# Performance work log

Measured on AMD Instinct MI355X. Metric: run time of the kernel, lower is better.

The kernel has to match this reference:

```python
import jax, jax.numpy as jnp
import numpy as np

B, C, H, W = 2, 192, 128, 128
DG, K = 4, 9  # deformable groups, kernel taps (3x3)


def conv3x3(x, w, b):
    y = jax.lax.conv_general_dilated(x, w, (1, 1), ((1, 1), (1, 1)),
                                     dimension_numbers=('NCHW', 'OIHW', 'NCHW'))
    return y + b[None, :, None, None]


def deform_sample(x, dy, dx, mask):
    # x: [B,C,H,W]; dy,dx,mask: [B,DG,K,H,W]. Returns [B,C,K,H,W] masked bilinear samples.
    b, c, h, w = x.shape
    cg = c // DG
    kk = jnp.arange(K)
    ky = (kk // 3 - 1).astype(x.dtype)  # kernel row offsets {-1,0,1}, pad=1, stride=1
    kx = (kk % 3 - 1).astype(x.dtype)
    ii = jnp.arange(h, dtype=x.dtype)
    jj = jnp.arange(w, dtype=x.dtype)
    py = ii[None, None, None, :, None] + ky[None, None, :, None, None] + dy  # [B,DG,K,H,W]
    px = jj[None, None, None, None, :] + kx[None, None, :, None, None] + dx
    y0 = jnp.floor(py)
    x0 = jnp.floor(px)
    ly = py - y0
    lx = px - x0
    xf = x.reshape(b, DG, cg, h * w)
    out = jnp.zeros((b, DG, cg, K, h, w), dtype=x.dtype)
    corners = [(y0, x0, (1 - ly) * (1 - lx)), (y0, x0 + 1, (1 - ly) * lx),
               (y0 + 1, x0, ly * (1 - lx)), (y0 + 1, x0 + 1, ly * lx)]
    for yc, xc, wt in corners:
        valid = (yc >= 0) & (yc < h) & (xc >= 0) & (xc < w)  # zero padding outside
        wv = wt * valid.astype(x.dtype)
        idx = (jnp.clip(yc, 0, h - 1) * w + jnp.clip(xc, 0, w - 1)).astype(jnp.int32)
        idxb = jnp.broadcast_to(idx.reshape(b, DG, 1, K * h * w), (b, DG, cg, K * h * w))
        g = jnp.take_along_axis(xf, idxb, axis=3).reshape(b, DG, cg, K, h, w)
        out = out + wv[:, :, None] * g
    out = out * mask[:, :, None]
    return out.reshape(b, c, K, h, w)


def setup_inputs() -> dict:
    key = jax.random.key(0)
    ks = jax.random.split(key, 8)
    f32 = jnp.float32
    x_vq = jax.random.normal(ks[0], (B, C, H, W), f32)
    x_residual = jax.random.normal(ks[1], (B, C, H, W), f32)
    w_off = jax.random.normal(ks[2], (C, 2 * C, 3, 3), f32) * (1.0 / np.sqrt(2 * C * 9))
    b_off = jnp.zeros((C,), f32)
    # conv_offset of DCNv2Pack: C -> 3*DG*K channels; small init keeps offsets moderate
    w_co = jax.random.normal(ks[3], (3 * DG * K, C, 3, 3), f32) * 0.02
    b_co = jnp.zeros((3 * DG * K,), f32)
    w_dcn = jax.random.normal(ks[4], (C, C, 3, 3), f32) * (1.0 / np.sqrt(C * 9))
    b_dcn = jnp.zeros((C,), f32)
    return {"x_vq": x_vq, "x_residual": x_residual, "w_off": w_off, "b_off": b_off,
            "w_co": w_co, "b_co": b_co, "w_dcn": w_dcn, "b_dcn": b_dcn}


def reference(x_vq, x_residual, w_off, b_off, w_co, b_co, w_dcn, b_dcn):
    feat = conv3x3(jnp.concatenate([x_vq, x_residual], axis=1), w_off, b_off)  # [B,C,H,W]
    off_out = conv3x3(feat, w_co, b_co)  # [B,3*DG*K,H,W]
    gk = DG * K
    o1 = off_out[:, :gk]
    o2 = off_out[:, gk:2 * gk]
    mask = jax.nn.sigmoid(off_out[:, 2 * gk:])
    dy = o1.reshape(B, DG, K, H, W)
    dx = o2.reshape(B, DG, K, H, W)
    m = mask.reshape(B, DG, K, H, W)
    sampled = deform_sample(x_vq, dy, dx, m)  # [B,C,K,H,W]
    y = jnp.einsum('ock,bckhw->bohw', w_dcn.reshape(C, C, K), sampled)
    return y + b_dcn[None, :, None, None]
```

## Files before the change

kernel.cpp:

```cpp
#include <hip/hip_runtime.h>
#include <hip/hip_bf16.h>
#include <math.h>

#define HH 128
#define WW 128
#define HW 16384
#define BB 2
#define CC 192

typedef __attribute__((ext_vector_type(8)))  short short8;
typedef __attribute__((ext_vector_type(4)))  float f32x4;
typedef __attribute__((ext_vector_type(16))) float f32x16;
typedef __attribute__((ext_vector_type(2)))  float f32x2;
typedef __attribute__((ext_vector_type(4)))  unsigned u32x4;

static __device__ __forceinline__ short f2bf(float f) {
    unsigned u = __float_as_uint(f);
    unsigned r = (u + 0x7FFFu + ((u >> 16) & 1u)) >> 16;
    return (short)r;
}
static __device__ __forceinline__ f32x2 unpk(unsigned u) {
    f32x2 r;
    r[0] = __uint_as_float(u << 16);
    r[1] = __uint_as_float(u & 0xFFFF0000u);
    return r;
}

static __device__ __forceinline__ void gl_lds16(const short* gsrc, short* ldst) {
    __builtin_amdgcn_global_load_lds(
        (const __attribute__((address_space(1))) unsigned*)gsrc,
        (__attribute__((address_space(3))) unsigned*)ldst, 16, 0, 0);
}

__global__ __launch_bounds__(256) void to_grp_k(
    const float* __restrict__ xv, const float* __restrict__ xr,
    unsigned short* __restrict__ xg)
{
    const int idx = blockIdx.x * 256 + threadIdx.x;
    const int pos = idx & (HW - 1);
    const int cgb = idx >> 14;
    const int cg  = cgb % 48;
    const int b   = cgb / 48;
    short8 v;
#pragma unroll
    for (int r = 0; r < 8; r++) {
        const int c = cg * 8 + r;
        const float f = (c < 192)
            ? xv[((size_t)(b * 192 + c) << 14) + pos]
            : xr[((size_t)(b * 192 + (c - 192)) << 14) + pos];
        v[r] = f2bf(f);
    }
    *reinterpret_cast<short8*>(xg + (size_t)idx * 8) = v;
}

__global__ void pack_w_k(const float* __restrict__ w, short* __restrict__ wp,
                         int Co, int so, int d1, int s1, int d2, int s2, int s3,
                         int total)
{
    const int idx = blockIdx.x * blockDim.x + threadIdx.x;
    if (idx >= total) return;
    const int lane  = idx & 63;
    const int slot  = (idx >> 6) & 7;
    const int chunk = idx >> 9;
    const int o     = slot * 32 + (lane & 31);
    const int k0    = chunk * 16 + ((lane >> 5) << 3);
    short8 v;
#pragma unroll
    for (int r = 0; r < 8; r++) {
        const int k = k0 + r;
        float f = 0.f;
        if (o < Co) {
            const int rem = k % d1;
            f = w[(size_t)o * so + (k / d1) * s1 + (rem / d2) * s2 + (rem % d2) * s3];
        }
        v[r] = f2bf(f);
    }
    *reinterpret_cast<short8*>(wp + (size_t)idx * 8) = v;
}

template<int MTW, int NC16, bool OUT_GRP>
__global__ __launch_bounds__(256, 2) void conv_g_k(
    const unsigned short* __restrict__ xg,
    const short* __restrict__ wA, const float* __restrict__ bias,
    void* __restrict__ outp, int Cout)
{
    __shared__ __align__(16) short Pbuf[3][2][4096];

    const int t    = threadIdx.x;
    const int lane = t & 63;
    const int wid  = t >> 6;
    const int mg   = wid >> 1;
    const int nt   = wid & 1;
    const int lin  = (blockIdx.z * HH + blockIdx.y) * 2 + blockIdx.x;
    const int og_  = (lin & 7) * 64 + (lin >> 3);
    const int j0   = (og_ & 1) * 64;
    const int i    = (og_ >> 1) & (HH - 1);
    const int b    = og_ >> 8;
    const int px   = j0 + (nt << 5) + (lane & 31);
    const int hi   = lane >> 5;
    constexpr int NQ = NC16 * 9;
    constexpr int NP = NQ / 2;

    const unsigned short* __restrict__ xgb = xg + (size_t)b * (NC16 * 2) * HW * 8;

    f32x16 acc[MTW];
#pragma unroll
    for (int m = 0; m < MTW; m++)
#pragma unroll
        for (int r = 0; r < 16; r++) acc[m][r] = 0.f;

    auto loadB = [&](int qq, short8& dst, bool& vm) {
        const int c16 = qq / 9;
        const int tap = qq - c16 * 9;
        const int iy  = i + tap / 3 - 1;
        const int jx  = px + tap % 3 - 1;
        vm = ((unsigned)iy < HH) && ((unsigned)jx < WW);
        const int iyc = min(max(iy, 0), HH - 1);
        const int jxc = min(max(jx, 0), WW - 1);
        dst = *reinterpret_cast<const short8*>(
            xgb + ((size_t)(c16 * 2 + hi) * HW + (iyc << 7) + jxc) * 8);
    };
    auto stage2 = [&](int chunk, int pb, int sl) {
        gl_lds16(wA + (size_t)chunk * 4096 + t * 8,         &Pbuf[pb][sl][wid * 512]);
        gl_lds16(wA + (size_t)chunk * 4096 + (t + 256) * 8, &Pbuf[pb][sl][2048 + wid * 512]);
    };

    short8 B0, B1, B2, B3, B4, B5;
    bool M0, M1, M2, M3, M4, M5;

    stage2(0, 0, 0); stage2(1, 0, 1);
    loadB(0, B0, M0); loadB(1, B1, M1);
    stage2(2, 1, 0); stage2(3, 1, 1);
    loadB(2, B2, M2); loadB(3, B3, M3);

#define CCHUNK(IBUF, SL, BC, MC)                                              \
    {                                                                         \
        short8 bF = BC;                                                       \
        if (!MC) {                                                            \
            _Pragma("unroll")                                                 \
            for (int r = 0; r < 8; r++) bF[r] = 0;                            \
        }                                                                     \
        const short* ab_ = &Pbuf[IBUF][SL][(mg * MTW) * 512 + lane * 8];      \
        short8 aF[MTW];                                                       \
        _Pragma("unroll")                                                     \
        for (int m = 0; m < MTW; m++)                                         \
            aF[m] = *reinterpret_cast<const short8*>(ab_ + m * 512);          \
        __builtin_amdgcn_s_setprio(1);                                        \
        _Pragma("unroll")                                                     \
        for (int m = 0; m < MTW; m++)                                         \
            acc[m] = __builtin_amdgcn_mfma_f32_32x32x16_bf16(aF[m], bF, acc[m], 0, 0, 0); \
        __builtin_amdgcn_s_setprio(0);                                        \
    }

#define PSTEP(P, IBUF, SBUF, Bc0, Mc0, Bc1, Mc1, Bn0, Mn0, Bn1, Mn1)          \
    {                                                                         \
        loadB(min(2 * ((P) + 2),     NQ - 1), Bn0, Mn0);                      \
        loadB(min(2 * ((P) + 2) + 1, NQ - 1), Bn1, Mn1);                      \
        asm volatile("s_waitcnt vmcnt(8)" ::: "memory");                      \
        __builtin_amdgcn_s_barrier();                                         \
        __builtin_amdgcn_sched_barrier(0);                                    \
        const int sc0_ = min(2 * ((P) + 2),     NQ - 1);                      \
        const int sc1_ = min(2 * ((P) + 2) + 1, NQ - 1);                      \
        stage2(sc0_, SBUF, 0); stage2(sc1_, SBUF, 1);                         \
        CCHUNK(IBUF, 0, Bc0, Mc0);                                            \
        CCHUNK(IBUF, 1, Bc1, Mc1);                                            \
    }

    for (int pp = 0; pp < NP; pp += 3) {
        PSTEP(pp + 0, 0, 2, B0, M0, B1, M1, B4, M4, B5, M5);
        PSTEP(pp + 1, 1, 0, B2, M2, B3, M3, B0, M0, B1, M1);
        PSTEP(pp + 2, 2, 1, B4, M4, B5, M5, B2, M2, B3, M3);
    }
#undef PSTEP
#undef CCHUNK

    const int pos_o = (i << 7) + px;
    if constexpr (OUT_GRP) {
        unsigned short* fg = (unsigned short*)outp;
#pragma unroll
        for (int m = 0; m < MTW; m++) {
            const int mt32 = mg * MTW + m;
#pragma unroll
            for (int g = 0; g < 4; g++) {
                const int ob = mt32 * 32 + 8 * g + 4 * hi;
                const unsigned s0 = (unsigned short)f2bf(acc[m][4 * g + 0] + bias[ob + 0]);
                const unsigned s1 = (unsigned short)f2bf(acc[m][4 * g + 1] + bias[ob + 1]);
                const unsigned s2 = (unsigned short)f2bf(acc[m][4 * g + 2] + bias[ob + 2]);
                const unsigned s3 = (unsigned short)f2bf(acc[m][4 * g + 3] + bias[ob + 3]);
                const int cg = mt32 * 4 + g;
                *reinterpret_cast<uint2*>(
                    fg + ((size_t)(b * (Cout >> 3) + cg) * HW + pos_o) * 8 + 4 * hi) =
                    make_uint2(s0 | (s1 << 16), s2 | (s3 << 16));
            }
        }
    } else {
        float* of = (float*)outp;
#pragma unroll
        for (int m = 0; m < MTW; m++) {
            const int mt32 = mg * MTW + m;
#pragma unroll
            for (int reg = 0; reg < 16; reg++) {
                const int o = mt32 * 32 + (reg & 3) + ((reg >> 2) << 3) + (hi << 2);
                if (o < Cout)
                    of[((size_t)(b * Cout + o) << 14) + pos_o] = acc[m][reg] + bias[o];
            }
        }
    }
}

__global__ __launch_bounds__(128, 2) void dcn_g_k(
    const unsigned short* __restrict__ xg, const float* __restrict__ off,
    const short* __restrict__ wA, const float* __restrict__ bias,
    float* __restrict__ out)
{
    __shared__ __align__(16) f32x4 eW[1152];
    __shared__ __align__(8)  uint2 eO[1152];
    __shared__ __align__(16) short bfS[2][2][512];

    const int t    = threadIdx.x;
    const int lane = t & 63;
    const int w    = t >> 6;
    const int lin  = (blockIdx.z * HH + blockIdx.y) * 4 + blockIdx.x;
    const int og_  = (lin & 7) * 128 + (lin >> 3);
    const int jt   = og_ & 3;
    const int i    = (og_ >> 2) & (HH - 1);
    const int b    = og_ >> 9;
    const int j0   = jt * 32;

    for (int e = t; e < 1152; e += 128) {
        const int p  = e & 31;
        const int gk = e >> 5;
        const int kt = gk % 9;
        const int j  = j0 + p;
        const size_t sp = (size_t)b * 108 * HW + (size_t)gk * HW + (i << 7) + j;
        const float dy = off[sp];
        const float dx = off[sp + (size_t)36 * HW];
        const float mv = off[sp + (size_t)72 * HW];
        const float m  = 1.f / (1.f + expf(-mv));
        const float py = (float)(i + kt / 3 - 1) + dy;
        const float px = (float)(j + kt % 3 - 1) + dx;
        const float y0f = floorf(py), x0f = floorf(px);
        const float ly = py - y0f, lx = px - x0f;
        const int y0 = (int)y0f, x0 = (int)x0f;
        const float vy0 = (y0 >= 0 && y0 < HH) ? 1.f : 0.f;
        const float vy1 = (y0 + 1 >= 0 && y0 + 1 < HH) ? 1.f : 0.f;
        const float vx0 = (x0 >= 0 && x0 < WW) ? 1.f : 0.f;
        const float vx1 = (x0 + 1 >= 0 && x0 + 1 < WW) ? 1.f : 0.f;
        f32x4 w4;
        w4[0] = (1.f - ly) * (1.f - lx) * m * vy0 * vx0;
        w4[1] = (1.f - ly) * lx         * m * vy0 * vx1;
        w4[2] = ly         * (1.f - lx) * m * vy1 * vx0;
        w4[3] = ly         * lx         * m * vy1 * vx1;
        const int yc0 = min(max(y0, 0), HH - 1);
        const int yc1 = min(max(y0 + 1, 0), HH - 1);
        const int xc0 = min(max(x0, 0), WW - 1);
        const int xc1 = min(max(x0 + 1, 0), WW - 1);
        eW[e] = w4;
        eO[e] = make_uint2((unsigned)((yc0 << 7) + xc0) | ((unsigned)((yc0 << 7) + xc1) << 16),
                           (unsigned)((yc1 << 7) + xc0) | ((unsigned)((yc1 << 7) + xc1) << 16));
    }
    __syncthreads();

    const int px_l = lane & 31;
    const int hi   = lane >> 5;
    const unsigned short* __restrict__ xgb = xg + (size_t)b * 48 * HW * 8;

    f32x16 acc[3];
#pragma unroll
    for (int m = 0; m < 3; m++)
#pragma unroll
        for (int r = 0; r < 16; r++) acc[m][r] = 0.f;

#define GISSUE(QQ, N0, N1, N2, N3, WN)                                        \
    {                                                                         \
        const int qn_   = min((QQ), 107);                                     \
        const int c16n_ = qn_ / 9;                                            \
        const int ktn_  = qn_ - 9 * c16n_;                                    \
        const int e_    = ((c16n_ / 3) * 9 + ktn_) * 32 + px_l;               \
        const uint2 o_  = eO[e_];                                             \
        WN = eW[e_];                                                          \
        const unsigned short* base_ = xgb + (size_t)(c16n_ * 2 + hi) * (HW * 8); \
        N0 = *reinterpret_cast<const u32x4*>(base_ + (size_t)(o_.x & 0xFFFFu) * 8); \
        N1 = *reinterpret_cast<const u32x4*>(base_ + (size_t)(o_.x >> 16) * 8);     \
        N2 = *reinterpret_cast<const u32x4*>(base_ + (size_t)(o_.y & 0xFFFFu) * 8); \
        N3 = *reinterpret_cast<const u32x4*>(base_ + (size_t)(o_.y >> 16) * 8);     \
    }

#define AISSUE(PP, DST)                                                       \
    {                                                                         \
        const short* a0_ = wA + (size_t)min(2 * (PP),     107) * 4096 + (w * 3) * 512 + lane * 8; \
        const short* a1_ = wA + (size_t)min(2 * (PP) + 1, 107) * 4096 + (w * 3) * 512 + lane * 8; \
        DST[0] = *reinterpret_cast<const short8*>(a0_);                       \
        DST[1] = *reinterpret_cast<const short8*>(a0_ + 512);                 \
        DST[2] = *reinterpret_cast<const short8*>(a0_ + 1024);                \
        DST[3] = *reinterpret_cast<const short8*>(a1_);                       \
        DST[4] = *reinterpret_cast<const short8*>(a1_ + 512);                 \
        DST[5] = *reinterpret_cast<const short8*>(a1_ + 1024);                \
    }

#define PAIRSTEP(P, Ac, C0, C1, C2, C3, WC, An, N0, N1, N2, N3, WN)           \
    {                                                                         \
        GISSUE(2 * ((P) + 1) + w, N0, N1, N2, N3, WN);                        \
        AISSUE((P) + 1, An);                                                  \
        asm volatile("s_waitcnt vmcnt(10)" ::: "memory");                     \
        u32x4 rv_;                                                            \
        _Pragma("unroll")                                                     \
        for (int jj = 0; jj < 4; jj++) {                                      \
            f32x2 v_ = WC[0] * unpk(C0[jj]) + WC[1] * unpk(C1[jj])            \
                     + WC[2] * unpk(C2[jj]) + WC[3] * unpk(C3[jj]);           \
            __hip_bfloat162 h2_ = __float22bfloat162_rn(make_float2(v_[0], v_[1])); \
            unsigned hu_; __builtin_memcpy(&hu_, &h2_, 4);                    \
            rv_[jj] = hu_;                                                    \
        }                                                                     \
        *reinterpret_cast<u32x4*>(&bfS[(P) & 1][w][lane * 8]) = rv_;          \
        asm volatile("s_waitcnt lgkmcnt(0)" ::: "memory");                    \
        __builtin_amdgcn_s_barrier();                                         \
        __builtin_amdgcn_sched_barrier(0);                                    \
        const short8 bf0_ = *reinterpret_cast<const short8*>(&bfS[(P) & 1][0][lane * 8]); \
        const short8 bf1_ = *reinterpret_cast<const short8*>(&bfS[(P) & 1][1][lane * 8]); \
        __builtin_amdgcn_s_setprio(1);                                        \
        acc[0] = __builtin_amdgcn_mfma_f32_32x32x16_bf16(Ac[0], bf0_, acc[0], 0, 0, 0); \
        acc[1] = __builtin_amdgcn_mfma_f32_32x32x16_bf16(Ac[1], bf0_, acc[1], 0, 0, 0); \
        acc[2] = __builtin_amdgcn_mfma_f32_32x32x16_bf16(Ac[2], bf0_, acc[2], 0, 0, 0); \
        acc[0] = __builtin_amdgcn_mfma_f32_32x32x16_bf16(Ac[3], bf1_, acc[0], 0, 0, 0); \
        acc[1] = __builtin_amdgcn_mfma_f32_32x32x16_bf16(Ac[4], bf1_, acc[1], 0, 0, 0); \
        acc[2] = __builtin_amdgcn_mfma_f32_32x32x16_bf16(Ac[5], bf1_, acc[2], 0, 0, 0); \
        __builtin_amdgcn_s_setprio(0);                                        \
    }

    short8 Aa[6], Ab[6];
    u32x4 Gx0, Gx1, Gx2, Gx3, Gy0, Gy1, Gy2, Gy3;
    f32x4 wGx, wGy;

    GISSUE(0 + w, Gx0, Gx1, Gx2, Gx3, wGx);
    AISSUE(0, Aa);

    for (int pr = 0; pr < 54; pr += 2) {
        PAIRSTEP(pr,     Aa, Gx0, Gx1, Gx2, Gx3, wGx, Ab, Gy0, Gy1, Gy2, Gy3, wGy);
        PAIRSTEP(pr + 1, Ab, Gy0, Gy1, Gy2, Gy3, wGy, Aa, Gx0, Gx1, Gx2, Gx3, wGx);
    }
#undef PAIRSTEP
#undef AISSUE
#undef GISSUE

    const int pos_o = (i << 7) + j0 + px_l;
#pragma unroll
    for (int m = 0; m < 3; m++) {
        const int mt32 = w * 3 + m;
#pragma unroll
        for (int reg = 0; reg < 16; reg++) {
            const int o = mt32 * 32 + (reg & 3) + ((reg >> 2) << 3) + (hi << 2);
            out[((size_t)(b * CC + o) << 14) + pos_o] = acc[m][reg] + bias[o];
        }
    }
}

extern "C" void kernel_launch(void* const* d_in, const int* in_sizes, int n_in,
                              void* d_out, int out_size, void* d_ws, size_t ws_size,
                              hipStream_t stream)
{
    const float* x_vq  = (const float*)d_in[0];
    const float* x_res = (const float*)d_in[1];
    const float* w_off = (const float*)d_in[2];
    const float* b_off = (const float*)d_in[3];
    const float* w_co  = (const float*)d_in[4];
    const float* b_co  = (const float*)d_in[5];
    const float* w_dcn = (const float*)d_in[6];
    const float* b_dcn = (const float*)d_in[7];
    float* out = (float*)d_out;

    char* ws = (char*)d_ws;
    unsigned short* xg = (unsigned short*)ws;
    const size_t xg_sz = (size_t)BB * 48 * HW * 8 * 2;
    unsigned short* fg = (unsigned short*)(ws + xg_sz);
    const size_t fg_sz = (size_t)BB * 24 * HW * 8 * 2;
    float* offb = (float*)(ws + xg_sz + fg_sz);
    const size_t offb_sz = (size_t)BB * 108 * HW * 4;
    short* wA1 = (short*)(ws + xg_sz + fg_sz + offb_sz);
    short* wA2 = wA1 + (size_t)216 * 4096;
    short* wA3 = wA2 + (size_t)108 * 4096;

    to_grp_k<<<dim3(BB * 48 * HW / 256), 256, 0, stream>>>(x_vq, x_res, xg);

    pack_w_k<<<(216 * 512 + 255) / 256, 256, 0, stream>>>(
        w_off, wA1, 192, 3456, 144, 144, 16, 1, 9, 216 * 512);
    pack_w_k<<<(108 * 512 + 255) / 256, 256, 0, stream>>>(
        w_co, wA2, 108, 1728, 144, 144, 16, 1, 9, 108 * 512);
    pack_w_k<<<(108 * 512 + 255) / 256, 256, 0, stream>>>(
        w_dcn, wA3, 192, 1728, 144, 144, 16, 1, 9, 108 * 512);

    conv_g_k<3, 24, true><<<dim3(2, HH, BB), 256, 0, stream>>>(xg, wA1, b_off, fg, 192);
    conv_g_k<2, 12, false><<<dim3(2, HH, BB), 256, 0, stream>>>(fg, wA2, b_co, offb, 108);
    dcn_g_k<<<dim3(4, HH, BB), 128, 0, stream>>>(xg, offb, wA3, b_dcn, out);
}
```

Measured before the change: 174.2 us.

## Stage conv input halo tile in LDS instead of per-tap global loads

```diff
diff --git a/kernel.cpp b/kernel.cpp
--- a/kernel.cpp
+++ b/kernel.cpp
@@ -26,7 +26,7 @@
     return r;
 }
 
-static __device__ __forceinline__ void gl_lds16(const short* gsrc, short* ldst) {
+static __device__ __forceinline__ void gl_lds16(const void* gsrc, void* ldst) {
     __builtin_amdgcn_global_load_lds(
         (const __attribute__((address_space(1))) unsigned*)gsrc,
         (__attribute__((address_space(3))) unsigned*)ldst, 16, 0, 0);
@@ -85,6 +85,7 @@
     void* __restrict__ outp, int Cout)
 {
     __shared__ __align__(16) short Pbuf[3][2][4096];
+    __shared__ __align__(16) short Btile[2][4096];
 
     const int t    = threadIdx.x;
     const int lane = t & 63;
@@ -96,12 +97,13 @@
     const int j0   = (og_ & 1) * 64;
     const int i    = (og_ >> 1) & (HH - 1);
     const int b    = og_ >> 8;
-    const int px   = j0 + (nt << 5) + (lane & 31);
+    const int pxw  = (nt << 5) + (lane & 31);
     const int hi   = lane >> 5;
     constexpr int NQ = NC16 * 9;
     constexpr int NP = NQ / 2;
 
     const unsigned short* __restrict__ xgb = xg + (size_t)b * (NC16 * 2) * HW * 8;
+    const char* __restrict__ xgc = (const char*)xgb;
 
     f32x16 acc[MTW];
 #pragma unroll
@@ -109,34 +111,45 @@
 #pragma unroll
         for (int r = 0; r < 16; r++) acc[m][r] = 0.f;
 
-    auto loadB = [&](int qq, short8& dst, bool& vm) {
-        const int c16 = qq / 9;
-        const int tap = qq - c16 * 9;
-        const int iy  = i + tap / 3 - 1;
-        const int jx  = px + tap % 3 - 1;
-        vm = ((unsigned)iy < HH) && ((unsigned)jx < WW);
-        const int iyc = min(max(iy, 0), HH - 1);
-        const int jxc = min(max(jx, 0), WW - 1);
-        dst = *reinterpret_cast<const short8*>(
-            xgb + ((size_t)(c16 * 2 + hi) * HW + (iyc << 7) + jxc) * 8);
+    int spat[2], hib[2];
+#pragma unroll
+    for (int p = 0; p < 2; p++) {
+        const int off = p * 4096 + t * 16;
+        int rn = off / 1056; rn = rn > 5 ? 5 : rn;
+        const int wi  = off - rn * 1056;
+        const int h_  = rn >= 3 ? 1 : 0;
+        const int row = rn - 3 * h_;
+        const int gy  = min(max(i - 1 + row, 0), HH - 1);
+        spat[p] = ((gy << 7) + j0 - 1) * 16 + wi;
+        hib[p]  = h_;
+    }
+    auto stageB = [&](int nb) {
+        char* dstb = (char*)&Btile[nb & 1][0];
+#pragma unroll
+        for (int p = 0; p < 2; p++) {
+            const char* src = xgc + (size_t)(nb * 2 + hib[p]) * (HW * 16) + spat[p];
+            gl_lds16(src, dstb + p * 4096 + wid * 1024);
+        }
     };
     auto stage2 = [&](int chunk, int pb, int sl) {
         gl_lds16(wA + (size_t)chunk * 4096 + t * 8,         &Pbuf[pb][sl][wid * 512]);
         gl_lds16(wA + (size_t)chunk * 4096 + (t + 256) * 8, &Pbuf[pb][sl][2048 + wid * 512]);
     };
 
-    short8 B0, B1, B2, B3, B4, B5;
-    bool M0, M1, M2, M3, M4, M5;
-
     stage2(0, 0, 0); stage2(1, 0, 1);
-    loadB(0, B0, M0); loadB(1, B1, M1);
+    stageB(0);
     stage2(2, 1, 0); stage2(3, 1, 1);
-    loadB(2, B2, M2); loadB(3, B3, M3);
-
-#define CCHUNK(IBUF, SL, BC, MC)                                              \
+
+#define CCHUNK(IBUF, SL, Q)                                                   \
     {                                                                         \
-        short8 bF = BC;                                                       \
-        if (!MC) {                                                            \
+        const int cc16_ = (Q) / 9;                                            \
+        const int tap_  = (Q) - 9 * cc16_;                                    \
+        const int dy_ = tap_ / 3, dx_ = tap_ % 3;                             \
+        const int iy_ = i + dy_ - 1;                                          \
+        const int jx_ = j0 + pxw + dx_ - 1;                                   \
+        short8 bF = *reinterpret_cast<const short8*>(                         \
+            &Btile[cc16_ & 1][(hi * 3 + dy_) * 528 + (pxw + dx_) * 8]);       \
+        if (!(((unsigned)iy_ < HH) && ((unsigned)jx_ < WW))) {                \
             _Pragma("unroll")                                                 \
             for (int r = 0; r < 8; r++) bF[r] = 0;                            \
         }                                                                     \
@@ -152,29 +165,30 @@
         __builtin_amdgcn_s_setprio(0);                                        \
     }
 
-#define PSTEP(P, IBUF, SBUF, Bc0, Mc0, Bc1, Mc1, Bn0, Mn0, Bn1, Mn1)          \
+#define PSTEP(P, IBUF, SBUF)                                                  \
     {                                                                         \
-        loadB(min(2 * ((P) + 2),     NQ - 1), Bn0, Mn0);                      \
-        loadB(min(2 * ((P) + 2) + 1, NQ - 1), Bn1, Mn1);                      \
-        asm volatile("s_waitcnt vmcnt(8)" ::: "memory");                      \
+        asm volatile("s_waitcnt vmcnt(4)" ::: "memory");                      \
         __builtin_amdgcn_s_barrier();                                         \
         __builtin_amdgcn_sched_barrier(0);                                    \
-        const int sc0_ = min(2 * ((P) + 2),     NQ - 1);                      \
-        const int sc1_ = min(2 * ((P) + 2) + 1, NQ - 1);                      \
-        stage2(sc0_, SBUF, 0); stage2(sc1_, SBUF, 1);                         \
-        CCHUNK(IBUF, 0, Bc0, Mc0);                                            \
-        CCHUNK(IBUF, 1, Bc1, Mc1);                                            \
+        const int q0_  = 2 * (P);                                             \
+        const int c16_ = q0_ / 9;                                             \
+        const int t0_  = q0_ - 9 * c16_;                                      \
+        if (t0_ == 1 || t0_ == 2) stageB(min(c16_ + 1, NC16 - 1));            \
+        stage2(min(2 * ((P) + 2),     NQ - 1), SBUF, 0);                      \
+        stage2(min(2 * ((P) + 2) + 1, NQ - 1), SBUF, 1);                      \
+        CCHUNK(IBUF, 0, q0_);                                                 \
+        CCHUNK(IBUF, 1, q0_ + 1);                                             \
     }
 
     for (int pp = 0; pp < NP; pp += 3) {
-        PSTEP(pp + 0, 0, 2, B0, M0, B1, M1, B4, M4, B5, M5);
-        PSTEP(pp + 1, 1, 0, B2, M2, B3, M3, B0, M0, B1, M1);
-        PSTEP(pp + 2, 2, 1, B4, M4, B5, M5, B2, M2, B3, M3);
+        PSTEP(pp + 0, 0, 2);
+        PSTEP(pp + 1, 1, 0);
+        PSTEP(pp + 2, 2, 1);
     }
 #undef PSTEP
 #undef CCHUNK
 
-    const int pos_o = (i << 7) + px;
+    const int pos_o = (i << 7) + j0 + pxw;
     if constexpr (OUT_GRP) {
         unsigned short* fg = (unsigned short*)outp;
 #pragma unroll
@@ -370,13 +384,13 @@
     float* out = (float*)d_out;
 
     char* ws = (char*)d_ws;
-    unsigned short* xg = (unsigned short*)ws;
+    unsigned short* xg = (unsigned short*)(ws + 256);
     const size_t xg_sz = (size_t)BB * 48 * HW * 8 * 2;
-    unsigned short* fg = (unsigned short*)(ws + xg_sz);
+    unsigned short* fg = (unsigned short*)(ws + 256 + xg_sz);
     const size_t fg_sz = (size_t)BB * 24 * HW * 8 * 2;
-    float* offb = (float*)(ws + xg_sz + fg_sz);
+    float* offb = (float*)(ws + 256 + xg_sz + fg_sz);
     const size_t offb_sz = (size_t)BB * 108 * HW * 4;
-    short* wA1 = (short*)(ws + xg_sz + fg_sz + offb_sz);
+    short* wA1 = (short*)(ws + 256 + xg_sz + fg_sz + offb_sz);
     short* wA2 = wA1 + (size_t)216 * 4096;
     short* wA3 = wA2 + (size_t)108 * 4096;
 
```

Result: slower. 205.4 us (+17.9%).

## Split conv blocks by output-channel half and shrink to 128 threads

Applied to the files above, without the earlier changes.

```diff
diff --git a/kernel.cpp b/kernel.cpp
--- a/kernel.cpp
+++ b/kernel.cpp
@@ -26,7 +26,7 @@
     return r;
 }
 
-static __device__ __forceinline__ void gl_lds16(const short* gsrc, short* ldst) {
+static __device__ __forceinline__ void gl_lds16(const void* gsrc, void* ldst) {
     __builtin_amdgcn_global_load_lds(
         (const __attribute__((address_space(1))) unsigned*)gsrc,
         (__attribute__((address_space(3))) unsigned*)ldst, 16, 0, 0);
@@ -55,13 +55,13 @@
 
 __global__ void pack_w_k(const float* __restrict__ w, short* __restrict__ wp,
                          int Co, int so, int d1, int s1, int d2, int s2, int s3,
-                         int total)
+                         int SLOTS, int total)
 {
     const int idx = blockIdx.x * blockDim.x + threadIdx.x;
     if (idx >= total) return;
     const int lane  = idx & 63;
-    const int slot  = (idx >> 6) & 7;
-    const int chunk = idx >> 9;
+    const int slot  = (idx >> 6) % SLOTS;
+    const int chunk = (idx >> 6) / SLOTS;
     const int o     = slot * 32 + (lane & 31);
     const int k0    = chunk * 16 + ((lane >> 5) << 3);
     short8 v;
@@ -79,25 +79,26 @@
 }
 
 template<int MTW, int NC16, bool OUT_GRP>
-__global__ __launch_bounds__(256, 2) void conv_g_k(
+__global__ __launch_bounds__(128, 2) void conv_g_k(
     const unsigned short* __restrict__ xg,
     const short* __restrict__ wA, const float* __restrict__ bias,
     void* __restrict__ outp, int Cout)
 {
-    __shared__ __align__(16) short Pbuf[3][2][4096];
+    constexpr int NPASS   = (MTW >= 3) ? 2 : 1;
+    constexpr int SLOT_SH = NPASS * 1024;
+    __shared__ __align__(16) short Pbuf[3][2][SLOT_SH];
 
     const int t    = threadIdx.x;
     const int lane = t & 63;
     const int wid  = t >> 6;
-    const int mg   = wid >> 1;
-    const int nt   = wid & 1;
-    const int lin  = (blockIdx.z * HH + blockIdx.y) * 2 + blockIdx.x;
-    const int og_  = (lin & 7) * 64 + (lin >> 3);
-    const int j0   = (og_ & 1) * 64;
-    const int i    = (og_ >> 1) & (HH - 1);
-    const int b    = og_ >> 8;
-    const int px   = j0 + (nt << 5) + (lane & 31);
-    const int hi   = lane >> 5;
+    const int lin   = (blockIdx.z * HH + blockIdx.y) * 4 + blockIdx.x;
+    const int og_   = (lin & 7) * 128 + (lin >> 3);
+    const int chalf = og_ & 1;
+    const int pxh   = (og_ >> 1) & 1;
+    const int i     = (og_ >> 2) & (HH - 1);
+    const int b     = og_ >> 9;
+    const int px    = pxh * 64 + (wid << 5) + (lane & 31);
+    const int hi    = lane >> 5;
     constexpr int NQ = NC16 * 9;
     constexpr int NP = NQ / 2;
 
@@ -120,17 +121,19 @@
         dst = *reinterpret_cast<const short8*>(
             xgb + ((size_t)(c16 * 2 + hi) * HW + (iyc << 7) + jxc) * 8);
     };
-    auto stage2 = [&](int chunk, int pb, int sl) {
-        gl_lds16(wA + (size_t)chunk * 4096 + t * 8,         &Pbuf[pb][sl][wid * 512]);
-        gl_lds16(wA + (size_t)chunk * 4096 + (t + 256) * 8, &Pbuf[pb][sl][2048 + wid * 512]);
+    auto stageA = [&](int chunk, int pb, int sl) {
+        const short* src = wA + (size_t)chunk * (2 * MTW * 512) + chalf * (MTW * 512);
+#pragma unroll
+        for (int p = 0; p < NPASS; p++)
+            gl_lds16(src + p * 1024 + t * 8, &Pbuf[pb][sl][p * 1024 + wid * 512]);
     };
 
     short8 B0, B1, B2, B3, B4, B5;
     bool M0, M1, M2, M3, M4, M5;
 
-    stage2(0, 0, 0); stage2(1, 0, 1);
+    stageA(0, 0, 0); stageA(1, 0, 1);
     loadB(0, B0, M0); loadB(1, B1, M1);
-    stage2(2, 1, 0); stage2(3, 1, 1);
+    stageA(2, 1, 0); stageA(3, 1, 1);
     loadB(2, B2, M2); loadB(3, B3, M3);
 
 #define CCHUNK(IBUF, SL, BC, MC)                                              \
@@ -140,7 +143,7 @@
             _Pragma("unroll")                                                 \
             for (int r = 0; r < 8; r++) bF[r] = 0;                            \
         }                                                                     \
-        const short* ab_ = &Pbuf[IBUF][SL][(mg * MTW) * 512 + lane * 8];      \
+        const short* ab_ = &Pbuf[IBUF][SL][lane * 8];                         \
         short8 aF[MTW];                                                       \
         _Pragma("unroll")                                                     \
         for (int m = 0; m < MTW; m++)                                         \
@@ -156,12 +159,15 @@
     {                                                                         \
         loadB(min(2 * ((P) + 2),     NQ - 1), Bn0, Mn0);                      \
         loadB(min(2 * ((P) + 2) + 1, NQ - 1), Bn1, Mn1);                      \
-        asm volatile("s_waitcnt vmcnt(8)" ::: "memory");                      \
+        if constexpr (NPASS == 2) {                                           \
+            asm volatile("s_waitcnt vmcnt(8)" ::: "memory");                  \
+        } else {                                                              \
+            asm volatile("s_waitcnt vmcnt(6)" ::: "memory");                  \
+        }                                                                     \
         __builtin_amdgcn_s_barrier();                                         \
         __builtin_amdgcn_sched_barrier(0);                                    \
-        const int sc0_ = min(2 * ((P) + 2),     NQ - 1);                      \
-        const int sc1_ = min(2 * ((P) + 2) + 1, NQ - 1);                      \
-        stage2(sc0_, SBUF, 0); stage2(sc1_, SBUF, 1);                         \
+        stageA(min(2 * ((P) + 2),     NQ - 1), SBUF, 0);                      \
+        stageA(min(2 * ((P) + 2) + 1, NQ - 1), SBUF, 1);                      \
         CCHUNK(IBUF, 0, Bc0, Mc0);                                            \
         CCHUNK(IBUF, 1, Bc1, Mc1);                                            \
     }
@@ -179,7 +185,7 @@
         unsigned short* fg = (unsigned short*)outp;
 #pragma unroll
         for (int m = 0; m < MTW; m++) {
-            const int mt32 = mg * MTW + m;
+            const int mt32 = chalf * MTW + m;
 #pragma unroll
             for (int g = 0; g < 4; g++) {
                 const int ob = mt32 * 32 + 8 * g + 4 * hi;
@@ -197,7 +203,7 @@
         float* of = (float*)outp;
 #pragma unroll
         for (int m = 0; m < MTW; m++) {
-            const int mt32 = mg * MTW + m;
+            const int mt32 = chalf * MTW + m;
 #pragma unroll
             for (int reg = 0; reg < 16; reg++) {
                 const int o = mt32 * 32 + (reg & 3) + ((reg >> 2) << 3) + (hi << 2);
@@ -314,7 +320,7 @@
         }                                                                     \
         *reinterpret_cast<u32x4*>(&bfS[(P) & 1][w][lane * 8]) = rv_;          \
         asm volatile("s_waitcnt lgkmcnt(0)" ::: "memory");                    \
-        __builtin_amdgcn_s_barrier();                                         \
+        __builtin_amdgcn_s_barrier();                                        \
         __builtin_amdgcn_sched_barrier(0);                                    \
         const short8 bf0_ = *reinterpret_cast<const short8*>(&bfS[(P) & 1][0][lane * 8]); \
         const short8 bf1_ = *reinterpret_cast<const short8*>(&bfS[(P) & 1][1][lane * 8]); \
@@ -377,19 +383,19 @@
     float* offb = (float*)(ws + xg_sz + fg_sz);
     const size_t offb_sz = (size_t)BB * 108 * HW * 4;
     short* wA1 = (short*)(ws + xg_sz + fg_sz + offb_sz);
-    short* wA2 = wA1 + (size_t)216 * 4096;
-    short* wA3 = wA2 + (size_t)108 * 4096;
+    short* wA2 = wA1 + (size_t)216 * 3072 + 512;
+    short* wA3 = wA2 + (size_t)108 * 2048;
 
     to_grp_k<<<dim3(BB * 48 * HW / 256), 256, 0, stream>>>(x_vq, x_res, xg);
 
-    pack_w_k<<<(216 * 512 + 255) / 256, 256, 0, stream>>>(
-        w_off, wA1, 192, 3456, 144, 144, 16, 1, 9, 216 * 512);
-    pack_w_k<<<(108 * 512 + 255) / 256, 256, 0, stream>>>(
-        w_co, wA2, 108, 1728, 144, 144, 16, 1, 9, 108 * 512);
-    pack_w_k<<<(108 * 512 + 255) / 256, 256, 0, stream>>>(
-        w_dcn, wA3, 192, 1728, 144, 144, 16, 1, 9, 108 * 512);
-
-    conv_g_k<3, 24, true><<<dim3(2, HH, BB), 256, 0, stream>>>(xg, wA1, b_off, fg, 192);
-    conv_g_k<2, 12, false><<<dim3(2, HH, BB), 256, 0, stream>>>(fg, wA2, b_co, offb, 108);
+    pack_w_k<<<(216 * 6 * 64 + 255) / 256, 256, 0, stream>>>(
+        w_off, wA1, 192, 3456, 144, 144, 16, 1, 9, 6, 216 * 6 * 64);
+    pack_w_k<<<(108 * 4 * 64 + 255) / 256, 256, 0, stream>>>(
+        w_co, wA2, 108, 1728, 144, 144, 16, 1, 9, 4, 108 * 4 * 64);
+    pack_w_k<<<(108 * 8 * 64 + 255) / 256, 256, 0, stream>>>(
+        w_dcn, wA3, 192, 1728, 144, 144, 16, 1, 9, 8, 108 * 8 * 64);
+
+    conv_g_k<3, 24, true><<<dim3(4, HH, BB), 128, 0, stream>>>(xg, wA1, b_off, fg, 192);
+    conv_g_k<2, 12, false><<<dim3(4, HH, BB), 128, 0, stream>>>(fg, wA2, b_co, offb, 108);
     dcn_g_k<<<dim3(4, HH, BB), 128, 0, stream>>>(xg, offb, wA3, b_dcn, out);
 }
```

Result: no change. 176.2 us (+1.1%).
